# Optimization experiments

Hardware: AMD Instinct MI355X
Metric: run time of the kernel (lower is better)

## Reference

```python
import jax, jax.numpy as jnp
import numpy as np

V, D, L, H, T, F = 32000, 1024, 8, 16, 128, 2816
DH = D // H
ROPE_BASE = 10000.0
EPS = 1e-5


def rmsnorm(x, w):
    return x * jax.lax.rsqrt(jnp.mean(x * x, axis=-1, keepdims=True) + EPS) * w


def rope_tables():
    inv = 1.0 / (ROPE_BASE ** (jnp.arange(0, DH, 2, dtype=jnp.float32) / DH))
    ang = jnp.arange(T, dtype=jnp.float32)[:, None] * inv[None, :]  # [T, DH//2]
    cos = jnp.concatenate([jnp.cos(ang), jnp.cos(ang)], axis=-1)    # [T, DH]
    sin = jnp.concatenate([jnp.sin(ang), jnp.sin(ang)], axis=-1)
    return cos, sin


def rotate_half(x):
    a, b = jnp.split(x, 2, axis=-1)
    return jnp.concatenate([-b, a], axis=-1)


def setup_inputs():
    key = jax.random.key(0)
    ks = jax.random.split(key, 9)
    s = 0.02
    return {
        'input_ids': jax.random.randint(ks[0], (1, T), 0, V),
        'emb': jax.random.normal(ks[1], (V, D), jnp.float32) * s,
        'Wq': jax.random.normal(ks[2], (L, D, D), jnp.float32) * s,
        'Wk': jax.random.normal(ks[3], (L, D, D), jnp.float32) * s,
        'Wv': jax.random.normal(ks[4], (L, D, D), jnp.float32) * s,
        'Wo': jax.random.normal(ks[5], (L, D, D), jnp.float32) * s,
        'Wg': jax.random.normal(ks[6], (L, D, F), jnp.float32) * s,
        'Wu': jax.random.normal(ks[7], (L, D, F), jnp.float32) * s,
        'Wd': jax.random.normal(ks[8], (L, F, D), jnp.float32) * s,
        'attn_norm': jnp.ones((L, D), jnp.float32),
        'ffn_norm': jnp.ones((L, D), jnp.float32),
        'norm_out': jnp.ones((D,), jnp.float32),
    }


def reference(input_ids, emb, Wq, Wk, Wv, Wo, Wg, Wu, Wd, attn_norm, ffn_norm, norm_out):
    cos, sin = rope_tables()
    ids = input_ids.reshape(-1)          # batch=1, as in the torch loop
    xs_emb = emb[ids]                    # [T, D] per-token embeddings
    scale = 1.0 / np.sqrt(DH).astype(np.float32)
    pos = jnp.arange(T)

    def token_step(cache, inp):
        kc, vc = cache                   # each [L, T, H, DH] paged KV cache
        x, t = inp                       # x: [D], t: scalar position
        c_t, s_t = cos[t], sin[t]        # [DH]
        pos_mask = pos <= t              # causal validity over cache slots

        def layer_step(h, per_layer):
            wq, wk, wv, wo, wg, wu, wd, an, fn, kc_l, vc_l = per_layer
            hn = rmsnorm(h, an)
            q = (hn @ wq).reshape(H, DH)
            k = (hn @ wk).reshape(H, DH)
            v = (hn @ wv).reshape(H, DH)
            q = q * c_t + rotate_half(q) * s_t
            k = k * c_t + rotate_half(k) * s_t
            kc_l = jax.lax.dynamic_update_slice(kc_l, k[None], (t, 0, 0))
            vc_l = jax.lax.dynamic_update_slice(vc_l, v[None], (t, 0, 0))
            scores = jnp.einsum('hd,thd->ht', q, kc_l) * scale   # [H, T]
            scores = jnp.where(pos_mask[None, :], scores, -1e9)
            attn = jax.nn.softmax(scores, axis=-1)
            o = jnp.einsum('ht,thd->hd', attn, vc_l).reshape(D) @ wo
            h = h + o
            hn2 = rmsnorm(h, fn)
            h = h + (jax.nn.silu(hn2 @ wg) * (hn2 @ wu)) @ wd
            return h, (kc_l, vc_l)

        x_out, (kc, vc) = jax.lax.scan(
            layer_step, x,
            (Wq, Wk, Wv, Wo, Wg, Wu, Wd, attn_norm, ffn_norm, kc, vc))
        return (kc, vc), x_out

    cache0 = (jnp.zeros((L, T, H, DH), jnp.float32),
              jnp.zeros((L, T, H, DH), jnp.float32))
    _, xs_out = jax.lax.scan(token_step, cache0, (xs_emb, pos))
    x_last = rmsnorm(xs_out[-1], norm_out)
    logits = emb @ x_last                # tied lm_head: [V]
    return logits
```

## Files before the change

kernel.cpp:

```cpp
#include <hip/hip_runtime.h>
#include <hip/hip_bf16.h>
#include <math.h>

namespace {
constexpr int V = 32000, D = 1024, L = 8, H = 16, T = 128, F = 2816, DH = 64;
constexpr float EPS = 1e-5f;
constexpr float SCALE = 0.125f;
constexpr int QKVN = 3 * D;
constexpr int GUN  = 2 * F;
constexpr int NP_Q = 4;
constexpr int NP_O = 8;
constexpr int NP_G = 4;
constexpr int NP_D = 11;
}

typedef __attribute__((ext_vector_type(8))) short short8;
typedef __attribute__((ext_vector_type(4))) float f32x4;

__device__ __forceinline__ unsigned short f2bf(float x) {
    union { float f; unsigned u; } v; v.f = x;
    unsigned r = v.u + 0x7FFFu + ((v.u >> 16) & 1u);
    return (unsigned short)(r >> 16);
}

__global__ void embed_rope_kernel(const int* __restrict__ ids, const float* __restrict__ emb,
                                  float* __restrict__ X,
                                  float* __restrict__ cosT, float* __restrict__ sinT) {
    int t = blockIdx.x, tid = threadIdx.x;
    int id = ids[t];
    ((float4*)(X + (size_t)t * D))[tid] = ((const float4*)(emb + (size_t)id * D))[tid];
    if (tid < 32) {
        float inv = powf(10000.0f, -(2.0f * (float)tid) / (float)DH);
        float ang = (float)t * inv;
        cosT[t * 32 + tid] = cosf(ang);
        sinT[t * 32 + tid] = sinf(ang);
    }
}

template<int NP, bool BF16OUT>
__launch_bounds__(256)
__global__ void rmsnorm_sum_kernel(float* __restrict__ X, const float* __restrict__ P,
                                   const float* __restrict__ w, void* __restrict__ Y) {
    int t = blockIdx.x, tid = threadIdx.x;
    float4 xv = ((float4*)(X + (size_t)t * D))[tid];
    #pragma unroll
    for (int c = 0; c < NP; ++c) {
        float4 pv = ((const float4*)(P + ((size_t)c * T + t) * D))[tid];
        xv.x += pv.x; xv.y += pv.y; xv.z += pv.z; xv.w += pv.w;
    }
    if (NP) ((float4*)(X + (size_t)t * D))[tid] = xv;
    float s = xv.x * xv.x + xv.y * xv.y + xv.z * xv.z + xv.w * xv.w;
    for (int o = 32; o >= 1; o >>= 1) s += __shfl_xor(s, o);
    __shared__ float red[4];
    if ((tid & 63) == 0) red[tid >> 6] = s;
    __syncthreads();
    float tot = red[0] + red[1] + red[2] + red[3];
    float r = rsqrtf(tot / (float)D + EPS);
    float4 wv = ((const float4*)w)[tid];
    if (BF16OUT) {
        ushort4 y;
        y.x = f2bf(xv.x * r * wv.x); y.y = f2bf(xv.y * r * wv.y);
        y.z = f2bf(xv.z * r * wv.z); y.w = f2bf(xv.w * r * wv.w);
        ((ushort4*)((unsigned short*)Y + (size_t)t * D))[tid] = y;
    } else {
        float4 y;
        y.x = xv.x * r * wv.x; y.y = xv.y * r * wv.y;
        y.z = xv.z * r * wv.z; y.w = xv.w * r * wv.w;
        ((float4*)((float*)Y + (size_t)t * D))[tid] = y;
    }
}

template<int CH>
__launch_bounds__(256)
__global__ void gemm64_kernel(const unsigned short* __restrict__ A, int lda,
                              const float* __restrict__ W0, const float* __restrict__ W1,
                              const float* __restrict__ W2, int ldw,
                              float* __restrict__ out, int ldo, int zColOff,
                              size_t chunkStride) {
    constexpr int STAGES = CH / 128;
    constexpr int LSTR = 136;
    __shared__ unsigned short Bst[2][64 * LSTR];
    const float* W = blockIdx.z == 0 ? W0 : (blockIdx.z == 1 ? W1 : W2);
    const int tid = threadIdx.x;
    const int wave = tid >> 6, lane = tid & 63;
    const int n0 = blockIdx.x * 64;
    const int k0 = blockIdx.y * CH;

    const int sc = tid & 63;
    const int so = tid >> 6;
    const float* wCol = W + (size_t)k0 * ldw + n0 + sc;
    unsigned short* wp = &Bst[0][sc * LSTR];

    const int lrow = lane & 15;
    const int lqo = lane >> 4;
    const unsigned short* aB = A + (size_t)lrow * lda + k0 + lqo * 8;
    const unsigned short* bRd = &Bst[0][(wave * 16 + lrow) * LSTR + lqo * 8];

    f32x4 acc[8] = {};
    float pre[32];

    auto ldst = [&](int s) {
        #pragma unroll
        for (int p = 0; p < 4; ++p) {
            const float* src = wCol + (size_t)(s * 128 + (so * 4 + p) * 8) * ldw;
            #pragma unroll
            for (int j = 0; j < 8; ++j) pre[p * 8 + j] = src[(size_t)j * ldw];
        }
    };
    auto wrst = [&](int buf) {
        #pragma unroll
        for (int p = 0; p < 4; ++p) {
            short8 bv;
            #pragma unroll
            for (int j = 0; j < 8; ++j) bv[j] = (short)f2bf(pre[p * 8 + j]);
            *(short8*)(wp + buf * (64 * LSTR) + (so * 4 + p) * 8) = bv;
        }
    };

    ldst(0);
    wrst(0);
    __syncthreads();

    #pragma unroll
    for (int s = 0; s < STAGES; ++s) {
        if (s + 1 < STAGES) ldst(s + 1);
        const unsigned short* rd = bRd + (s & 1) * (64 * LSTR);
        #pragma unroll
        for (int ks = 0; ks < 4; ++ks) {
            short8 b = *(const short8*)(rd + ks * 32);
            #pragma unroll
            for (int mf = 0; mf < 8; ++mf) {
                short8 a = *(const short8*)(aB + (size_t)(mf * 16) * lda + s * 128 + ks * 32);
                acc[mf] = __builtin_amdgcn_mfma_f32_16x16x32_bf16(a, b, acc[mf], 0, 0, 0);
            }
        }
        if (s + 1 < STAGES) {
            __syncthreads();
            wrst((s + 1) & 1);
            __syncthreads();
        }
    }

    const int col = zColOff * blockIdx.z + n0 + wave * 16 + lrow;
    float* op = out + blockIdx.y * chunkStride;
    #pragma unroll
    for (int mf = 0; mf < 8; ++mf) {
        int r0 = mf * 16 + lqo * 4;
        #pragma unroll
        for (int r = 0; r < 4; ++r)
            op[(size_t)(r0 + r) * ldo + col] = acc[mf][r];
    }
}

__launch_bounds__(256)
__global__ void rope_reduce_kernel(const float* __restrict__ P,
                                   const float* __restrict__ cosT, const float* __restrict__ sinT,
                                   float* __restrict__ Qr, float* __restrict__ Kr,
                                   float* __restrict__ Vr) {
    int t = blockIdx.x, tid = threadIdx.x;
    int d0 = tid * 4;
    float4 q = {0.f, 0.f, 0.f, 0.f}, k = q, v = q;
    #pragma unroll
    for (int c = 0; c < NP_Q; ++c) {
        const float* base = P + ((size_t)c * T + t) * QKVN;
        float4 a = ((const float4*)base)[tid];
        float4 b = ((const float4*)(base + D))[tid];
        float4 w = ((const float4*)(base + 2 * D))[tid];
        q.x += a.x; q.y += a.y; q.z += a.z; q.w += a.w;
        k.x += b.x; k.y += b.y; k.z += b.z; k.w += b.w;
        v.x += w.x; v.y += w.y; v.z += w.z; v.w += w.w;
    }
    float4 c4 = *(const float4*)(cosT + t * 32 + (d0 & 31));
    float4 s4 = *(const float4*)(sinT + t * 32 + (d0 & 31));
    float sgn = (d0 & 32) ? 1.f : -1.f;
    float4 qp, kp;
    qp.x = __shfl_xor(q.x, 8); qp.y = __shfl_xor(q.y, 8);
    qp.z = __shfl_xor(q.z, 8); qp.w = __shfl_xor(q.w, 8);
    kp.x = __shfl_xor(k.x, 8); kp.y = __shfl_xor(k.y, 8);
    kp.z = __shfl_xor(k.z, 8); kp.w = __shfl_xor(k.w, 8);
    float4 qo, ko;
    qo.x = q.x * c4.x + sgn * qp.x * s4.x; qo.y = q.y * c4.y + sgn * qp.y * s4.y;
    qo.z = q.z * c4.z + sgn * qp.z * s4.z; qo.w = q.w * c4.w + sgn * qp.w * s4.w;
    ko.x = k.x * c4.x + sgn * kp.x * s4.x; ko.y = k.y * c4.y + sgn * kp.y * s4.y;
    ko.z = k.z * c4.z + sgn * kp.z * s4.z; ko.w = k.w * c4.w + sgn * kp.w * s4.w;
    ((float4*)(Qr + (size_t)t * D))[tid] = qo;
    ((float4*)(Kr + (size_t)t * D))[tid] = ko;
    ((float4*)(Vr + (size_t)t * D))[tid] = v;
}

__global__ void attn_kernel(const float* __restrict__ Q, const float* __restrict__ Kc,
                            const float* __restrict__ Vc, unsigned short* __restrict__ AO) {
    int t = blockIdx.x, h = blockIdx.y, lane = threadIdx.x;
    __shared__ float q[DH];
    __shared__ float p[T];
    q[lane] = Q[(size_t)t * D + h * DH + lane];
    __syncthreads();
    int j0 = lane, j1 = lane + 64;
    float s0 = -1e30f, s1 = -1e30f;
    if (j0 <= t) {
        const float* kr = Kc + (size_t)j0 * D + h * DH;
        float s = 0.f;
        #pragma unroll
        for (int d = 0; d < DH; ++d) s += q[d] * kr[d];
        s0 = s * SCALE;
    }
    if (j1 <= t) {
        const float* kr = Kc + (size_t)j1 * D + h * DH;
        float s = 0.f;
        #pragma unroll
        for (int d = 0; d < DH; ++d) s += q[d] * kr[d];
        s1 = s * SCALE;
    }
    float m = fmaxf(s0, s1);
    for (int o = 32; o >= 1; o >>= 1) m = fmaxf(m, __shfl_xor(m, o));
    float e0 = (j0 <= t) ? __expf(s0 - m) : 0.f;
    float e1 = (j1 <= t) ? __expf(s1 - m) : 0.f;
    float sum = e0 + e1;
    for (int o = 32; o >= 1; o >>= 1) sum += __shfl_xor(sum, o);
    float inv = 1.f / sum;
    p[j0] = e0 * inv;
    p[j1] = e1 * inv;
    __syncthreads();
    float acc = 0.f;
    const float* vcol = Vc + h * DH + lane;
    for (int j = 0; j <= t; ++j) acc += p[j] * vcol[(size_t)j * D];
    AO[(size_t)t * D + h * DH + lane] = f2bf(acc);
}

__launch_bounds__(256)
__global__ void silu_reduce_kernel(const float* __restrict__ P,
                                   unsigned short* __restrict__ Gact) {
    int t = blockIdx.y;
    int f = blockIdx.x * 256 + threadIdx.x;
    float g = 0.f, u = 0.f;
    #pragma unroll
    for (int c = 0; c < NP_G; ++c) {
        const float* base = P + ((size_t)c * T + t) * GUN;
        g += base[f];
        u += base[F + f];
    }
    Gact[(size_t)t * F + f] = f2bf(g / (1.f + __expf(-g)) * u);
}

__global__ void logits_kernel(const float* __restrict__ emb, const float* __restrict__ xl,
                              float* __restrict__ out) {
    __shared__ float x[D];
    int tid = threadIdx.x;
    ((float4*)x)[tid] = ((const float4*)xl)[tid];
    __syncthreads();
    int row = blockIdx.x * 4 + (tid >> 6);
    int lane = tid & 63;
    const float4* e4 = (const float4*)(emb + (size_t)row * D);
    const float4* x4 = (const float4*)x;
    float s = 0.f;
    #pragma unroll
    for (int k = lane; k < D / 4; k += 64) {
        float4 ev = e4[k], xv = x4[k];
        s += ev.x * xv.x + ev.y * xv.y + ev.z * xv.z + ev.w * xv.w;
    }
    for (int o = 32; o >= 1; o >>= 1) s += __shfl_xor(s, o);
    if (lane == 0) out[row] = s;
}

extern "C" void kernel_launch(void* const* d_in, const int* in_sizes, int n_in,
                              void* d_out, int out_size, void* d_ws, size_t ws_size,
                              hipStream_t stream) {
    const int*   ids = (const int*)d_in[0];
    const float* emb = (const float*)d_in[1];
    const float* Wq  = (const float*)d_in[2];
    const float* Wk  = (const float*)d_in[3];
    const float* Wv  = (const float*)d_in[4];
    const float* Wo  = (const float*)d_in[5];
    const float* Wg  = (const float*)d_in[6];
    const float* Wu  = (const float*)d_in[7];
    const float* Wd  = (const float*)d_in[8];
    const float* attn_norm = (const float*)d_in[9];
    const float* ffn_norm  = (const float*)d_in[10];
    const float* norm_out  = (const float*)d_in[11];
    float* out = (float*)d_out;

    size_t off = 0;
    auto alloc = [&](size_t bytes) {
        void* p = (char*)d_ws + off;
        off += (bytes + 255) & ~(size_t)255;
        return p;
    };
    float*          X     = (float*)alloc((size_t)T * D * 4);
    float*          P0    = (float*)alloc((size_t)NP_Q * T * QKVN * 4);
    float*          P1    = (float*)alloc((size_t)NP_O * T * D * 4);
    float*          P2    = (float*)alloc((size_t)NP_D * T * D * 4);
    float*          P3    = (float*)alloc((size_t)NP_G * T * GUN * 4);
    float*          Qr    = (float*)alloc((size_t)T * D * 4);
    float*          Kr    = (float*)alloc((size_t)T * D * 4);
    float*          Vr    = (float*)alloc((size_t)T * D * 4);
    float*          cosT  = (float*)alloc((size_t)T * 32 * 4);
    float*          sinT  = (float*)alloc((size_t)T * 32 * 4);
    float*          xl    = (float*)alloc((size_t)D * 4);
    unsigned short* Hn_bf = (unsigned short*)alloc((size_t)T * D * 2);
    unsigned short* AO_bf = (unsigned short*)alloc((size_t)T * D * 2);
    unsigned short* Gact  = (unsigned short*)alloc((size_t)T * F * 2);
    (void)ws_size;

    embed_rope_kernel<<<T, 256, 0, stream>>>(ids, emb, X, cosT, sinT);

    for (int l = 0; l < L; ++l) {
        const float* wq = Wq + (size_t)l * D * D;
        const float* wk = Wk + (size_t)l * D * D;
        const float* wv = Wv + (size_t)l * D * D;
        const float* wo = Wo + (size_t)l * D * D;
        const float* wg = Wg + (size_t)l * D * F;
        const float* wu = Wu + (size_t)l * D * F;
        const float* wd = Wd + (size_t)l * F * D;

        if (l == 0)
            rmsnorm_sum_kernel<0, true><<<T, 256, 0, stream>>>(
                X, P2, attn_norm + (size_t)l * D, Hn_bf);
        else
            rmsnorm_sum_kernel<NP_D, true><<<T, 256, 0, stream>>>(
                X, P2, attn_norm + (size_t)l * D, Hn_bf);
        gemm64_kernel<256><<<dim3(D / 64, NP_Q, 3), 256, 0, stream>>>(
            Hn_bf, D, wq, wk, wv, D, P0, QKVN, D, (size_t)T * QKVN);
        rope_reduce_kernel<<<T, 256, 0, stream>>>(P0, cosT, sinT, Qr, Kr, Vr);
        attn_kernel<<<dim3(T, H), 64, 0, stream>>>(Qr, Kr, Vr, AO_bf);
        gemm64_kernel<128><<<dim3(D / 64, NP_O, 1), 256, 0, stream>>>(
            AO_bf, D, wo, wo, wo, D, P1, D, 0, (size_t)T * D);
        rmsnorm_sum_kernel<NP_O, true><<<T, 256, 0, stream>>>(
            X, P1, ffn_norm + (size_t)l * D, Hn_bf);
        gemm64_kernel<256><<<dim3(F / 64, NP_G, 2), 256, 0, stream>>>(
            Hn_bf, D, wg, wu, wu, F, P3, GUN, F, (size_t)T * GUN);
        silu_reduce_kernel<<<dim3(F / 256, T), 256, 0, stream>>>(P3, Gact);
        gemm64_kernel<256><<<dim3(D / 64, NP_D, 1), 256, 0, stream>>>(
            Gact, F, wd, wd, wd, D, P2, D, 0, (size_t)T * D);
    }

    rmsnorm_sum_kernel<NP_D, false><<<1, 256, 0, stream>>>(
        X + (size_t)(T - 1) * D, P2 + (size_t)(T - 1) * D, norm_out, xl);
    logits_kernel<<<V / 4, 256, 0, stream>>>(emb, xl, out);
}
```

Before: 815.6 us.

## Fuse split-K reductions into QKV and gate/up GEMMs, fold RoPE into attention

Replaces the split-K QKV GEMM plus rope_reduce kernel with a single GEMM that splits K across the four waves of a block and reduces through shared memory. RoPE is now applied inside the attention kernel, with K rotated on the fly for each key. The gate/up GEMM likewise reduces in-block and applies SiLU*up directly, which removes the partial-sum buffers and two kernel launches per layer. In exchange, the new GEMMs use 16-column tiles and load weights straight from global memory without LDS staging. Attention also redoes the K rotation for every query.

```diff
diff --git a/kernel.cpp b/kernel.cpp
--- a/kernel.cpp
+++ b/kernel.cpp
@@ -7,10 +7,7 @@
 constexpr float EPS = 1e-5f;
 constexpr float SCALE = 0.125f;
 constexpr int QKVN = 3 * D;
-constexpr int GUN  = 2 * F;
-constexpr int NP_Q = 4;
 constexpr int NP_O = 8;
-constexpr int NP_G = 4;
 constexpr int NP_D = 11;
 }
 
@@ -70,35 +67,155 @@
     }
 }
 
+__launch_bounds__(256)
+__global__ void gemm_qkv_kernel(const unsigned short* __restrict__ A,
+                                const float* __restrict__ Wq, const float* __restrict__ Wk,
+                                const float* __restrict__ Wv, float* __restrict__ QKV) {
+    __shared__ float Ls[4][128][17];
+    const int tid = threadIdx.x, wave = tid >> 6, lane = tid & 63;
+    const int lrow = lane & 15, lqo = lane >> 4;
+    const int n16 = blockIdx.x * 16;
+    const int z = n16 >> 10;
+    const float* W = z == 0 ? Wq : (z == 1 ? Wk : Wv);
+    const int n0 = n16 & 1023;
+    const int k0 = wave * 256;
+    const unsigned short* aB = A + (size_t)lrow * D + k0 + lqo * 8;
+    const float* wB = W + (size_t)(k0 + lqo * 8) * D + n0 + lrow;
+    f32x4 acc[8] = {};
+    #pragma unroll
+    for (int half = 0; half < 2; ++half) {
+        float pre[32];
+        #pragma unroll
+        for (int ks = 0; ks < 4; ++ks)
+            #pragma unroll
+            for (int j = 0; j < 8; ++j)
+                pre[ks * 8 + j] = wB[(size_t)((half * 4 + ks) * 32 + j) * D];
+        #pragma unroll
+        for (int ks = 0; ks < 4; ++ks) {
+            short8 b;
+            #pragma unroll
+            for (int j = 0; j < 8; ++j) b[j] = (short)f2bf(pre[ks * 8 + j]);
+            #pragma unroll
+            for (int mf = 0; mf < 8; ++mf) {
+                short8 a = *(const short8*)(aB + (size_t)(mf * 16) * D + (half * 4 + ks) * 32);
+                acc[mf] = __builtin_amdgcn_mfma_f32_16x16x32_bf16(a, b, acc[mf], 0, 0, 0);
+            }
+        }
+    }
+    #pragma unroll
+    for (int mf = 0; mf < 8; ++mf)
+        #pragma unroll
+        for (int r = 0; r < 4; ++r)
+            Ls[wave][mf * 16 + lqo * 4 + r][lrow] = acc[mf][r];
+    __syncthreads();
+    #pragma unroll
+    for (int m2 = 0; m2 < 2; ++m2)
+        #pragma unroll
+        for (int r = 0; r < 4; ++r) {
+            int row = (wave * 2 + m2) * 16 + lqo * 4 + r;
+            float v = Ls[0][row][lrow] + Ls[1][row][lrow] +
+                      Ls[2][row][lrow] + Ls[3][row][lrow];
+            QKV[(size_t)row * QKVN + n16 + lrow] = v;
+        }
+}
+
+__launch_bounds__(256)
+__global__ void gemm_gusilu_kernel(const unsigned short* __restrict__ A,
+                                   const float* __restrict__ Wg, const float* __restrict__ Wu,
+                                   unsigned short* __restrict__ Gact) {
+    __shared__ float Ls[4][128][17];
+    const int tid = threadIdx.x, wave = tid >> 6, lane = tid & 63;
+    const int lrow = lane & 15, lqo = lane >> 4;
+    const int n0 = blockIdx.x * 16;
+    const int k0 = wave * 256;
+    const unsigned short* aB = A + (size_t)lrow * D + k0 + lqo * 8;
+    const float* gB = Wg + (size_t)(k0 + lqo * 8) * F + n0 + lrow;
+    const float* uB = Wu + (size_t)(k0 + lqo * 8) * F + n0 + lrow;
+    f32x4 aG[8] = {}, aU[8] = {};
+    #pragma unroll
+    for (int half = 0; half < 2; ++half) {
+        float pg[32], pu[32];
+        #pragma unroll
+        for (int ks = 0; ks < 4; ++ks)
+            #pragma unroll
+            for (int j = 0; j < 8; ++j) {
+                size_t roff = (size_t)((half * 4 + ks) * 32 + j) * F;
+                pg[ks * 8 + j] = gB[roff];
+                pu[ks * 8 + j] = uB[roff];
+            }
+        #pragma unroll
+        for (int ks = 0; ks < 4; ++ks) {
+            short8 bg, bu;
+            #pragma unroll
+            for (int j = 0; j < 8; ++j) {
+                bg[j] = (short)f2bf(pg[ks * 8 + j]);
+                bu[j] = (short)f2bf(pu[ks * 8 + j]);
+            }
+            #pragma unroll
+            for (int mf = 0; mf < 8; ++mf) {
+                short8 a = *(const short8*)(aB + (size_t)(mf * 16) * D + (half * 4 + ks) * 32);
+                aG[mf] = __builtin_amdgcn_mfma_f32_16x16x32_bf16(a, bg, aG[mf], 0, 0, 0);
+                aU[mf] = __builtin_amdgcn_mfma_f32_16x16x32_bf16(a, bu, aU[mf], 0, 0, 0);
+            }
+        }
+    }
+    #pragma unroll
+    for (int mf = 0; mf < 8; ++mf)
+        #pragma unroll
+        for (int r = 0; r < 4; ++r)
+            Ls[wave][mf * 16 + lqo * 4 + r][lrow] = aG[mf][r];
+    __syncthreads();
+    float gs[8];
+    #pragma unroll
+    for (int m2 = 0; m2 < 2; ++m2)
+        #pragma unroll
+        for (int r = 0; r < 4; ++r) {
+            int row = (wave * 2 + m2) * 16 + lqo * 4 + r;
+            gs[m2 * 4 + r] = Ls[0][row][lrow] + Ls[1][row][lrow] +
+                             Ls[2][row][lrow] + Ls[3][row][lrow];
+        }
+    __syncthreads();
+    #pragma unroll
+    for (int mf = 0; mf < 8; ++mf)
+        #pragma unroll
+        for (int r = 0; r < 4; ++r)
+            Ls[wave][mf * 16 + lqo * 4 + r][lrow] = aU[mf][r];
+    __syncthreads();
+    #pragma unroll
+    for (int m2 = 0; m2 < 2; ++m2)
+        #pragma unroll
+        for (int r = 0; r < 4; ++r) {
+            int row = (wave * 2 + m2) * 16 + lqo * 4 + r;
+            float us = Ls[0][row][lrow] + Ls[1][row][lrow] +
+                       Ls[2][row][lrow] + Ls[3][row][lrow];
+            float g = gs[m2 * 4 + r];
+            Gact[(size_t)row * F + n0 + lrow] = f2bf(g / (1.f + __expf(-g)) * us);
+        }
+}
+
 template<int CH>
 __launch_bounds__(256)
 __global__ void gemm64_kernel(const unsigned short* __restrict__ A, int lda,
-                              const float* __restrict__ W0, const float* __restrict__ W1,
-                              const float* __restrict__ W2, int ldw,
-                              float* __restrict__ out, int ldo, int zColOff,
+                              const float* __restrict__ W, int ldw,
+                              float* __restrict__ out, int ldo,
                               size_t chunkStride) {
     constexpr int STAGES = CH / 128;
     constexpr int LSTR = 136;
     __shared__ unsigned short Bst[2][64 * LSTR];
-    const float* W = blockIdx.z == 0 ? W0 : (blockIdx.z == 1 ? W1 : W2);
     const int tid = threadIdx.x;
     const int wave = tid >> 6, lane = tid & 63;
     const int n0 = blockIdx.x * 64;
     const int k0 = blockIdx.y * CH;
-
     const int sc = tid & 63;
     const int so = tid >> 6;
     const float* wCol = W + (size_t)k0 * ldw + n0 + sc;
     unsigned short* wp = &Bst[0][sc * LSTR];
-
     const int lrow = lane & 15;
     const int lqo = lane >> 4;
     const unsigned short* aB = A + (size_t)lrow * lda + k0 + lqo * 8;
     const unsigned short* bRd = &Bst[0][(wave * 16 + lrow) * LSTR + lqo * 8];
-
     f32x4 acc[8] = {};
     float pre[32];
-
     auto ldst = [&](int s) {
         #pragma unroll
         for (int p = 0; p < 4; ++p) {
@@ -116,11 +233,9 @@
             *(short8*)(wp + buf * (64 * LSTR) + (so * 4 + p) * 8) = bv;
         }
     };
-
     ldst(0);
     wrst(0);
     __syncthreads();
-
     #pragma unroll
     for (int s = 0; s < STAGES; ++s) {
         if (s + 1 < STAGES) ldst(s + 1);
@@ -140,8 +255,7 @@
             __syncthreads();
         }
     }
-
-    const int col = zColOff * blockIdx.z + n0 + wave * 16 + lrow;
+    const int col = n0 + wave * 16 + lrow;
     float* op = out + blockIdx.y * chunkStride;
     #pragma unroll
     for (int mf = 0; mf < 8; ++mf) {
@@ -152,63 +266,46 @@
     }
 }
 
-__launch_bounds__(256)
-__global__ void rope_reduce_kernel(const float* __restrict__ P,
-                                   const float* __restrict__ cosT, const float* __restrict__ sinT,
-                                   float* __restrict__ Qr, float* __restrict__ Kr,
-                                   float* __restrict__ Vr) {
-    int t = blockIdx.x, tid = threadIdx.x;
-    int d0 = tid * 4;
-    float4 q = {0.f, 0.f, 0.f, 0.f}, k = q, v = q;
-    #pragma unroll
-    for (int c = 0; c < NP_Q; ++c) {
-        const float* base = P + ((size_t)c * T + t) * QKVN;
-        float4 a = ((const float4*)base)[tid];
-        float4 b = ((const float4*)(base + D))[tid];
-        float4 w = ((const float4*)(base + 2 * D))[tid];
-        q.x += a.x; q.y += a.y; q.z += a.z; q.w += a.w;
-        k.x += b.x; k.y += b.y; k.z += b.z; k.w += b.w;
-        v.x += w.x; v.y += w.y; v.z += w.z; v.w += w.w;
-    }
-    float4 c4 = *(const float4*)(cosT + t * 32 + (d0 & 31));
-    float4 s4 = *(const float4*)(sinT + t * 32 + (d0 & 31));
-    float sgn = (d0 & 32) ? 1.f : -1.f;
-    float4 qp, kp;
-    qp.x = __shfl_xor(q.x, 8); qp.y = __shfl_xor(q.y, 8);
-    qp.z = __shfl_xor(q.z, 8); qp.w = __shfl_xor(q.w, 8);
-    kp.x = __shfl_xor(k.x, 8); kp.y = __shfl_xor(k.y, 8);
-    kp.z = __shfl_xor(k.z, 8); kp.w = __shfl_xor(k.w, 8);
-    float4 qo, ko;
-    qo.x = q.x * c4.x + sgn * qp.x * s4.x; qo.y = q.y * c4.y + sgn * qp.y * s4.y;
-    qo.z = q.z * c4.z + sgn * qp.z * s4.z; qo.w = q.w * c4.w + sgn * qp.w * s4.w;
-    ko.x = k.x * c4.x + sgn * kp.x * s4.x; ko.y = k.y * c4.y + sgn * kp.y * s4.y;
-    ko.z = k.z * c4.z + sgn * kp.z * s4.z; ko.w = k.w * c4.w + sgn * kp.w * s4.w;
-    ((float4*)(Qr + (size_t)t * D))[tid] = qo;
-    ((float4*)(Kr + (size_t)t * D))[tid] = ko;
-    ((float4*)(Vr + (size_t)t * D))[tid] = v;
-}
-
-__global__ void attn_kernel(const float* __restrict__ Q, const float* __restrict__ Kc,
-                            const float* __restrict__ Vc, unsigned short* __restrict__ AO) {
+__global__ void attn_rope_kernel(const float* __restrict__ QKV,
+                                 const float* __restrict__ cosT, const float* __restrict__ sinT,
+                                 unsigned short* __restrict__ AO) {
     int t = blockIdx.x, h = blockIdx.y, lane = threadIdx.x;
     __shared__ float q[DH];
     __shared__ float p[T];
-    q[lane] = Q[(size_t)t * D + h * DH + lane];
+    float qv = QKV[(size_t)t * QKVN + h * DH + lane];
+    float qpart = __shfl_xor(qv, 32);
+    {
+        int i = lane & 31;
+        float c = cosT[t * 32 + i], sn = sinT[t * 32 + i];
+        q[lane] = (lane < 32) ? (qv * c - qpart * sn) : (qv * c + qpart * sn);
+    }
     __syncthreads();
     int j0 = lane, j1 = lane + 64;
     float s0 = -1e30f, s1 = -1e30f;
     if (j0 <= t) {
-        const float* kr = Kc + (size_t)j0 * D + h * DH;
+        const float* kr = QKV + (size_t)j0 * QKVN + D + h * DH;
+        const float* cr = cosT + j0 * 32;
+        const float* sr = sinT + j0 * 32;
         float s = 0.f;
-        #pragma unroll
-        for (int d = 0; d < DH; ++d) s += q[d] * kr[d];
+        #pragma unroll 8
+        for (int d = 0; d < 32; ++d) {
+            float ka = kr[d], kb = kr[d + 32];
+            float c = cr[d], sn = sr[d];
+            s += q[d] * (ka * c - kb * sn) + q[d + 32] * (kb * c + ka * sn);
+        }
         s0 = s * SCALE;
     }
     if (j1 <= t) {
-        const float* kr = Kc + (size_t)j1 * D + h * DH;
+        const float* kr = QKV + (size_t)j1 * QKVN + D + h * DH;
+        const float* cr = cosT + j1 * 32;
+        const float* sr = sinT + j1 * 32;
         float s = 0.f;
-        #pragma unroll
-        for (int d = 0; d < DH; ++d) s += q[d] * kr[d];
+        #pragma unroll 8
+        for (int d = 0; d < 32; ++d) {
+            float ka = kr[d], kb = kr[d + 32];
+            float c = cr[d], sn = sr[d];
+            s += q[d] * (ka * c - kb * sn) + q[d + 32] * (kb * c + ka * sn);
+        }
         s1 = s * SCALE;
     }
     float m = fmaxf(s0, s1);
@@ -222,24 +319,9 @@
     p[j1] = e1 * inv;
     __syncthreads();
     float acc = 0.f;
-    const float* vcol = Vc + h * DH + lane;
-    for (int j = 0; j <= t; ++j) acc += p[j] * vcol[(size_t)j * D];
+    const float* vcol = QKV + 2 * D + h * DH + lane;
+    for (int j = 0; j <= t; ++j) acc += p[j] * vcol[(size_t)j * QKVN];
     AO[(size_t)t * D + h * DH + lane] = f2bf(acc);
-}
-
-__launch_bounds__(256)
-__global__ void silu_reduce_kernel(const float* __restrict__ P,
-                                   unsigned short* __restrict__ Gact) {
-    int t = blockIdx.y;
-    int f = blockIdx.x * 256 + threadIdx.x;
-    float g = 0.f, u = 0.f;
-    #pragma unroll
-    for (int c = 0; c < NP_G; ++c) {
-        const float* base = P + ((size_t)c * T + t) * GUN;
-        g += base[f];
-        u += base[F + f];
-    }
-    Gact[(size_t)t * F + f] = f2bf(g / (1.f + __expf(-g)) * u);
 }
 
 __global__ void logits_kernel(const float* __restrict__ emb, const float* __restrict__ xl,
@@ -286,13 +368,9 @@
         return p;
     };
     float*          X     = (float*)alloc((size_t)T * D * 4);
-    float*          P0    = (float*)alloc((size_t)NP_Q * T * QKVN * 4);
+    float*          QKV   = (float*)alloc((size_t)T * QKVN * 4);
     float*          P1    = (float*)alloc((size_t)NP_O * T * D * 4);
     float*          P2    = (float*)alloc((size_t)NP_D * T * D * 4);
-    float*          P3    = (float*)alloc((size_t)NP_G * T * GUN * 4);
-    float*          Qr    = (float*)alloc((size_t)T * D * 4);
-    float*          Kr    = (float*)alloc((size_t)T * D * 4);
-    float*          Vr    = (float*)alloc((size_t)T * D * 4);
     float*          cosT  = (float*)alloc((size_t)T * 32 * 4);
     float*          sinT  = (float*)alloc((size_t)T * 32 * 4);
     float*          xl    = (float*)alloc((size_t)D * 4);
@@ -318,19 +396,15 @@
         else
             rmsnorm_sum_kernel<NP_D, true><<<T, 256, 0, stream>>>(
                 X, P2, attn_norm + (size_t)l * D, Hn_bf);
-        gemm64_kernel<256><<<dim3(D / 64, NP_Q, 3), 256, 0, stream>>>(
-            Hn_bf, D, wq, wk, wv, D, P0, QKVN, D, (size_t)T * QKVN);
-        rope_reduce_kernel<<<T, 256, 0, stream>>>(P0, cosT, sinT, Qr, Kr, Vr);
-        attn_kernel<<<dim3(T, H), 64, 0, stream>>>(Qr, Kr, Vr, AO_bf);
-        gemm64_kernel<128><<<dim3(D / 64, NP_O, 1), 256, 0, stream>>>(
-            AO_bf, D, wo, wo, wo, D, P1, D, 0, (size_t)T * D);
+        gemm_qkv_kernel<<<QKVN / 16, 256, 0, stream>>>(Hn_bf, wq, wk, wv, QKV);
+        attn_rope_kernel<<<dim3(T, H), 64, 0, stream>>>(QKV, cosT, sinT, AO_bf);
+        gemm64_kernel<128><<<dim3(D / 64, NP_O), 256, 0, stream>>>(
+            AO_bf, D, wo, D, P1, D, (size_t)T * D);
         rmsnorm_sum_kernel<NP_O, true><<<T, 256, 0, stream>>>(
             X, P1, ffn_norm + (size_t)l * D, Hn_bf);
-        gemm64_kernel<256><<<dim3(F / 64, NP_G, 2), 256, 0, stream>>>(
-            Hn_bf, D, wg, wu, wu, F, P3, GUN, F, (size_t)T * GUN);
-        silu_reduce_kernel<<<dim3(F / 256, T), 256, 0, stream>>>(P3, Gact);
-        gemm64_kernel<256><<<dim3(D / 64, NP_D, 1), 256, 0, stream>>>(
-            Gact, F, wd, wd, wd, D, P2, D, 0, (size_t)T * D);
+        gemm_gusilu_kernel<<<F / 16, 256, 0, stream>>>(Hn_bf, wg, wu, Gact);
+        gemm64_kernel<256><<<dim3(D / 64, NP_D), 256, 0, stream>>>(
+            Gact, F, wd, D, P2, D, (size_t)T * D);
     }
 
     rmsnorm_sum_kernel<NP_D, false><<<1, 256, 0, stream>>>(
```

New measurement: 921.1 us. 12.9% more time.
